# Kernel tuning notes

Hardware: AMD Instinct MI355X
Metric: run time of the kernel (lower is better)

The kernel has to match this reference:

```python
import jax, jax.numpy as jnp
from jax import lax
import numpy as np

GRID = 256   # spatial_shape of the sparse voxel volume (D=H=W)
N_ACTIVE = 500000
K = 5        # kernel_size=5, padding=2, stride=1 -> 'same' box-sum conv


def setup_inputs() -> dict:
    key = jax.random.key(0)
    k1, k2 = jax.random.split(key)
    feats = jax.random.normal(k1, (N_ACTIVE,), dtype=jnp.float32)
    coords = jax.random.randint(k2, (N_ACTIVE, 3), 0, GRID, dtype=jnp.int32)
    return {"feats": feats, "coords": coords}


def reference(feats, coords):
    # Densify the sparse tensor: scatter active-voxel features into [B=1, C=1, D, H, W].
    vol = jnp.zeros((1, 1, GRID, GRID, GRID), dtype=feats.dtype)
    vol = vol.at[0, 0, coords[:, 0], coords[:, 1], coords[:, 2]].add(feats)
    # Frozen all-ones 5x5x5 kernel (weight.data = ones, requires_grad=False), no bias.
    kernel = jnp.ones((1, 1, K, K, K), dtype=feats.dtype)  # OIDHW
    pad = K // 2
    out = lax.conv_general_dilated(
        vol, kernel,
        window_strides=(1, 1, 1),
        padding=[(pad, pad)] * 3,
        dimension_numbers=("NCDHW", "OIDHW", "NCDHW"),
    )
    # Original returns a list of one dense volume; return the array.
    return out
```

## Files before the change

kernel.cpp:

```cpp
#include <hip/hip_runtime.h>

#define GRIDN 256
#define NVOX (GRIDN * GRIDN * GRIDN)
#define NYT  16
#define NBKT (GRIDN * NYT)
#define BCAP 512

typedef float floatx4 __attribute__((ext_vector_type(4)));

__global__ __launch_bounds__(256) void k_bin(const float* __restrict__ feats,
                                             const int* __restrict__ coords,
                                             int* __restrict__ cnt,
                                             int2* __restrict__ rec, int n) {
    int i = blockIdx.x * blockDim.x + threadIdx.x;
    if (i >= n) return;
    int d = coords[3 * i + 0];
    int h = coords[3 * i + 1];
    int w = coords[3 * i + 2];
    int key = d * NYT + (h >> 4);
    int slot = atomicAdd(&cnt[key], 1);
    if (slot < BCAP)
        rec[(size_t)key * BCAP + slot] = make_int2(w | (h << 8), __float_as_int(feats[i]));
}

#define TXF 64
#define TYF 16
#define ZS  8
__global__ __launch_bounds__(256) void k_fused_sparse(const int* __restrict__ cnt,
                                                      const int2* __restrict__ rec,
                                                      float* __restrict__ out) {
    __shared__ float Xp[2][TYF + 4][64];

    const int tid = threadIdx.x;
    int wg  = blockIdx.x;
    int swz = (wg & 7) * 256 + (wg >> 3);
    const int x0 = (swz & 3) * TXF;
    const int y0 = ((swz >> 2) & 15) * TYF;
    const int z0 = (swz >> 6) * ZS;

    const int xq = (tid & 15) * 4;
    const int yy = tid >> 4;
    const int yt_lo = max(0, (y0 - 2) >> 4);
    const int yt_hi = min(NYT - 1, (y0 + TYF + 1) >> 4);

    for (int idx = tid; idx < 2 * (TYF + 4) * 16; idx += 256)
        ((float4*)Xp)[idx] = make_float4(0.f, 0.f, 0.f, 0.f);

    float4 a0 = {0,0,0,0}, a1 = {0,0,0,0}, a2 = {0,0,0,0},
           a3 = {0,0,0,0}, a4 = {0,0,0,0};

    for (int zi = z0 - 2; zi < z0 + ZS + 2; ++zi) {
        const int cb = zi & 1;
        __syncthreads();
        if ((unsigned)zi < (unsigned)GRIDN) {
            for (int yt = yt_lo; yt <= yt_hi; ++yt) {
                int b  = zi * NYT + yt;
                int nb = min(cnt[b], BCAP);
                const int2* rb = rec + (size_t)b * BCAP;
                for (int j = tid; j < nb; j += 256) {
                    int2 r = rb[j];
                    int x  = r.x & 255;
                    int y  = (r.x >> 8) & 255;
                    int ry = y - y0 + 2;
                    int cx = x - x0;
                    if ((unsigned)ry < (unsigned)(TYF + 4) && (unsigned)(cx + 2) < 68u) {
                        float f = __int_as_float(r.y);
                        #pragma unroll
                        for (int dx = -2; dx <= 2; ++dx) {
                            int cc = cx + dx;
                            if ((unsigned)cc < 64u)
                                atomicAdd(&Xp[cb][ry][cc], f);
                        }
                    }
                }
            }
        }
        __syncthreads();
        float4 q0 = *(const float4*)&Xp[cb][yy + 0][xq];
        float4 q1 = *(const float4*)&Xp[cb][yy + 1][xq];
        float4 q2 = *(const float4*)&Xp[cb][yy + 2][xq];
        float4 q3 = *(const float4*)&Xp[cb][yy + 3][xq];
        float4 q4 = *(const float4*)&Xp[cb][yy + 4][xq];
        float4 v;
        v.x = q0.x + q1.x + q2.x + q3.x + q4.x;
        v.y = q0.y + q1.y + q2.y + q3.y + q4.y;
        v.z = q0.z + q1.z + q2.z + q3.z + q4.z;
        v.w = q0.w + q1.w + q2.w + q3.w + q4.w;
        for (int idx = tid; idx < (TYF + 4) * 16; idx += 256)
            ((float4*)Xp[cb ^ 1])[idx] = make_float4(0.f, 0.f, 0.f, 0.f);
        a0 = a1; a1 = a2; a2 = a3; a3 = a4; a4 = v;
        int zo = zi - 2;
        if (zo >= z0) {
            float4 s;
            s.x = a0.x + a1.x + a2.x + a3.x + a4.x;
            s.y = a0.y + a1.y + a2.y + a3.y + a4.y;
            s.z = a0.z + a1.z + a2.z + a3.z + a4.z;
            s.w = a0.w + a1.w + a2.w + a3.w + a4.w;
            float4* op = (float4*)(out + (size_t)zo * (GRIDN * GRIDN)
                                       + (size_t)(y0 + yy) * GRIDN + x0 + xq);
            *op = s;
        }
    }
}

__global__ __launch_bounds__(256) void k_zero4(floatx4* __restrict__ p, int n4) {
    int stride = gridDim.x * blockDim.x;
    floatx4 z = {0.f, 0.f, 0.f, 0.f};
    for (int i = blockIdx.x * blockDim.x + threadIdx.x; i < n4; i += stride)
        __builtin_nontemporal_store(z, &p[i]);
}

__global__ void k_scatter125(const float* __restrict__ feats,
                             const int* __restrict__ coords,
                             float* __restrict__ out, int n) {
    int i = blockIdx.x * blockDim.x + threadIdx.x;
    if (i >= n) return;
    int d = coords[3 * i + 0];
    int h = coords[3 * i + 1];
    int w = coords[3 * i + 2];
    float f = feats[i];
    int d0 = max(d - 2, 0), d1 = min(d + 2, GRIDN - 1);
    int h0 = max(h - 2, 0), h1 = min(h + 2, GRIDN - 1);
    int w0 = max(w - 2, 0), w1 = min(w + 2, GRIDN - 1);
    for (int dd = d0; dd <= d1; ++dd)
        for (int hh = h0; hh <= h1; ++hh)
            for (int ww = w0; ww <= w1; ++ww)
                atomicAdd(&out[(dd * GRIDN + hh) * GRIDN + ww], f);
}

extern "C" void kernel_launch(void* const* d_in, const int* in_sizes, int n_in,
                              void* d_out, int out_size, void* d_ws, size_t ws_size,
                              hipStream_t stream) {
    const float* feats  = (const float*)d_in[0];
    const int*   coords = (const int*)d_in[1];
    float*       out    = (float*)d_out;
    int n = in_sizes[0];

    const size_t cnt_bytes = (size_t)NBKT * sizeof(int);
    const size_t rec_bytes = (size_t)NBKT * BCAP * sizeof(int2);

    if (ws_size >= cnt_bytes + rec_bytes) {
        int*  cnt = (int*)d_ws;
        int2* rec = (int2*)((char*)d_ws + cnt_bytes);
        hipMemsetAsync(cnt, 0, cnt_bytes, stream);
        k_bin<<<(n + 255) / 256, 256, 0, stream>>>(feats, coords, cnt, rec, n);
        k_fused_sparse<<<2048, 256, 0, stream>>>(cnt, rec, out);
    } else {
        k_zero4<<<4096, 256, 0, stream>>>((floatx4*)out, NVOX / 4);
        k_scatter125<<<(n + 255) / 256, 256, 0, stream>>>(feats, coords, out, n);
    }
}
```

Measured before the change: 90.99 us.

## Prefetch next z-slice bucket records and pad bucket counters to separate lines

The counts for the bucket records of all 36 (z-slice, y-tile) buckets are loaded into shared memory once per block. The records of the 3 y-tile buckets in a slice are then flattened into one list, and the next slice's records are loaded into registers while the current slice is scattered, so global load latency overlaps the LDS atomics. Bucket counters are spaced 32 ints apart to reduce atomic contention on shared cache lines, which increases the memset size. Record writes and the final output writes use nontemporal stores.

```diff
diff --git a/kernel.cpp b/kernel.cpp
--- a/kernel.cpp
+++ b/kernel.cpp
@@ -5,8 +5,10 @@
 #define NYT  16
 #define NBKT (GRIDN * NYT)
 #define BCAP 512
+#define CSTR 32
 
 typedef float floatx4 __attribute__((ext_vector_type(4)));
+typedef int   intx2   __attribute__((ext_vector_type(2)));
 
 __global__ __launch_bounds__(256) void k_bin(const float* __restrict__ feats,
                                              const int* __restrict__ coords,
@@ -18,9 +20,13 @@
     int h = coords[3 * i + 1];
     int w = coords[3 * i + 2];
     int key = d * NYT + (h >> 4);
-    int slot = atomicAdd(&cnt[key], 1);
-    if (slot < BCAP)
-        rec[(size_t)key * BCAP + slot] = make_int2(w | (h << 8), __float_as_int(feats[i]));
+    int slot = atomicAdd(&cnt[key * CSTR], 1);
+    if (slot < BCAP) {
+        intx2 r;
+        r.x = w | (h << 8);
+        r.y = __float_as_int(feats[i]);
+        __builtin_nontemporal_store(r, (intx2*)&rec[(size_t)key * BCAP + slot]);
+    }
 }
 
 #define TXF 64
@@ -30,6 +36,8 @@
                                                       const int2* __restrict__ rec,
                                                       float* __restrict__ out) {
     __shared__ float Xp[2][TYF + 4][64];
+    __shared__ int   cm[12][3];
+    __shared__ int   cb_[12][3];
 
     const int tid = threadIdx.x;
     int wg  = blockIdx.x;
@@ -38,68 +46,102 @@
     const int y0 = ((swz >> 2) & 15) * TYF;
     const int z0 = (swz >> 6) * ZS;
 
-    const int xq = (tid & 15) * 4;
-    const int yy = tid >> 4;
-    const int yt_lo = max(0, (y0 - 2) >> 4);
-    const int yt_hi = min(NYT - 1, (y0 + TYF + 1) >> 4);
+    const int xq  = (tid & 15) * 4;
+    const int yy  = tid >> 4;
+    const int yt0 = y0 >> 4;
 
+    if (tid < 36) {
+        int k  = tid / 3, t = tid - 3 * k;
+        int zi = z0 - 2 + k;
+        int yt = yt0 - 1 + t;
+        int m = 0, b = -1;
+        if ((unsigned)zi < (unsigned)GRIDN && (unsigned)yt < (unsigned)NYT) {
+            b = zi * NYT + yt;
+            m = min(cnt[b * CSTR], BCAP);
+        }
+        cm[k][t]  = m;
+        cb_[k][t] = b;
+    }
     for (int idx = tid; idx < 2 * (TYF + 4) * 16; idx += 256)
         ((float4*)Xp)[idx] = make_float4(0.f, 0.f, 0.f, 0.f);
+    __syncthreads();
+
+    auto load_rec = [&](int k, int j) -> int2 {
+        int m0 = cm[k][0], m1 = cm[k][1];
+        int b, s;
+        if (j < m0)           { b = cb_[k][0]; s = j; }
+        else if (j < m0 + m1) { b = cb_[k][1]; s = j - m0; }
+        else                  { b = cb_[k][2]; s = j - m0 - m1; }
+        return rec[(size_t)b * BCAP + s];
+    };
+
+    int2 p0 = {0, 0}, p1 = {0, 0};
+    {
+        int M = cm[0][0] + cm[0][1] + cm[0][2];
+        if (tid < M)       p0 = load_rec(0, tid);
+        if (tid + 256 < M) p1 = load_rec(0, tid + 256);
+    }
 
     float4 a0 = {0,0,0,0}, a1 = {0,0,0,0}, a2 = {0,0,0,0},
            a3 = {0,0,0,0}, a4 = {0,0,0,0};
 
-    for (int zi = z0 - 2; zi < z0 + ZS + 2; ++zi) {
-        const int cb = zi & 1;
+    for (int k = 0; k < ZS + 4; ++k) {
+        const int cbuf = k & 1;
         __syncthreads();
-        if ((unsigned)zi < (unsigned)GRIDN) {
-            for (int yt = yt_lo; yt <= yt_hi; ++yt) {
-                int b  = zi * NYT + yt;
-                int nb = min(cnt[b], BCAP);
-                const int2* rb = rec + (size_t)b * BCAP;
-                for (int j = tid; j < nb; j += 256) {
-                    int2 r = rb[j];
-                    int x  = r.x & 255;
-                    int y  = (r.x >> 8) & 255;
-                    int ry = y - y0 + 2;
-                    int cx = x - x0;
-                    if ((unsigned)ry < (unsigned)(TYF + 4) && (unsigned)(cx + 2) < 68u) {
-                        float f = __int_as_float(r.y);
-                        #pragma unroll
-                        for (int dx = -2; dx <= 2; ++dx) {
-                            int cc = cx + dx;
-                            if ((unsigned)cc < 64u)
-                                atomicAdd(&Xp[cb][ry][cc], f);
-                        }
+        int2 q0 = {0, 0}, q1 = {0, 0};
+        if (k + 1 < ZS + 4) {
+            int Mn = cm[k + 1][0] + cm[k + 1][1] + cm[k + 1][2];
+            if (tid < Mn)       q0 = load_rec(k + 1, tid);
+            if (tid + 256 < Mn) q1 = load_rec(k + 1, tid + 256);
+        }
+        const int M = cm[k][0] + cm[k][1] + cm[k][2];
+        {
+            auto scat = [&](int2 r) {
+                int x  = r.x & 255;
+                int y  = (r.x >> 8) & 255;
+                int ry = y - y0 + 2;
+                int cx = x - x0;
+                if ((unsigned)ry < (unsigned)(TYF + 4) && (unsigned)(cx + 2) < 68u) {
+                    float f = __int_as_float(r.y);
+                    #pragma unroll
+                    for (int dx = -2; dx <= 2; ++dx) {
+                        int cc = cx + dx;
+                        if ((unsigned)cc < 64u)
+                            atomicAdd(&Xp[cbuf][ry][cc], f);
                     }
                 }
-            }
+            };
+            if (tid < M)       scat(p0);
+            if (tid + 256 < M) scat(p1);
+            for (int j = tid + 512; j < M; j += 256)
+                scat(load_rec(k, j));
         }
         __syncthreads();
-        float4 q0 = *(const float4*)&Xp[cb][yy + 0][xq];
-        float4 q1 = *(const float4*)&Xp[cb][yy + 1][xq];
-        float4 q2 = *(const float4*)&Xp[cb][yy + 2][xq];
-        float4 q3 = *(const float4*)&Xp[cb][yy + 3][xq];
-        float4 q4 = *(const float4*)&Xp[cb][yy + 4][xq];
+        float4 q0r = *(const float4*)&Xp[cbuf][yy + 0][xq];
+        float4 q1r = *(const float4*)&Xp[cbuf][yy + 1][xq];
+        float4 q2r = *(const float4*)&Xp[cbuf][yy + 2][xq];
+        float4 q3r = *(const float4*)&Xp[cbuf][yy + 3][xq];
+        float4 q4r = *(const float4*)&Xp[cbuf][yy + 4][xq];
         float4 v;
-        v.x = q0.x + q1.x + q2.x + q3.x + q4.x;
-        v.y = q0.y + q1.y + q2.y + q3.y + q4.y;
-        v.z = q0.z + q1.z + q2.z + q3.z + q4.z;
-        v.w = q0.w + q1.w + q2.w + q3.w + q4.w;
+        v.x = q0r.x + q1r.x + q2r.x + q3r.x + q4r.x;
+        v.y = q0r.y + q1r.y + q2r.y + q3r.y + q4r.y;
+        v.z = q0r.z + q1r.z + q2r.z + q3r.z + q4r.z;
+        v.w = q0r.w + q1r.w + q2r.w + q3r.w + q4r.w;
         for (int idx = tid; idx < (TYF + 4) * 16; idx += 256)
-            ((float4*)Xp[cb ^ 1])[idx] = make_float4(0.f, 0.f, 0.f, 0.f);
+            ((float4*)Xp[cbuf ^ 1])[idx] = make_float4(0.f, 0.f, 0.f, 0.f);
         a0 = a1; a1 = a2; a2 = a3; a3 = a4; a4 = v;
-        int zo = zi - 2;
-        if (zo >= z0) {
-            float4 s;
+        int zo = z0 + k - 4;
+        if (k >= 4) {
+            floatx4 s;
             s.x = a0.x + a1.x + a2.x + a3.x + a4.x;
             s.y = a0.y + a1.y + a2.y + a3.y + a4.y;
             s.z = a0.z + a1.z + a2.z + a3.z + a4.z;
             s.w = a0.w + a1.w + a2.w + a3.w + a4.w;
-            float4* op = (float4*)(out + (size_t)zo * (GRIDN * GRIDN)
-                                       + (size_t)(y0 + yy) * GRIDN + x0 + xq);
-            *op = s;
+            floatx4* op = (floatx4*)(out + (size_t)zo * (GRIDN * GRIDN)
+                                         + (size_t)(y0 + yy) * GRIDN + x0 + xq);
+            __builtin_nontemporal_store(s, op);
         }
+        p0 = q0; p1 = q1;
     }
 }
 
@@ -136,7 +178,7 @@
     float*       out    = (float*)d_out;
     int n = in_sizes[0];
 
-    const size_t cnt_bytes = (size_t)NBKT * sizeof(int);
+    const size_t cnt_bytes = (size_t)NBKT * CSTR * sizeof(int);
     const size_t rec_bytes = (size_t)NBKT * BCAP * sizeof(int2);
 
     if (ws_size >= cnt_bytes + rec_bytes) {
```

Result: faster. 82.16 us (-9.7%).
